# Kernel tuning notes

Hardware: AMD Instinct MI355X
Metric: run time of the kernel (lower is better)

Reference implementation:

```python
import jax, jax.numpy as jnp
import numpy as np

N = 100000      # num nodes
E = 3200000     # num edges
F = 128         # feature dim (in == out, required by final in-place copy)
U = 1000        # num_users


def gcn_conv(x, edge_index, W, b):
    """PyG GCNConv: symmetric-normalized adjacency with self-loops.
    out = D^{-1/2} (A + I) D^{-1/2} X W + b
    """
    xw = x @ W                                   # [N, F]
    src, dst = edge_index[0], edge_index[1]
    # in-degree including the self-loop (+1)
    deg = jax.ops.segment_sum(jnp.ones((E,), x.dtype), dst, num_segments=N) + 1.0
    inv_sqrt = jax.lax.rsqrt(deg)                # [N]
    coef = inv_sqrt[src] * inv_sqrt[dst]         # [E]
    agg = jax.ops.segment_sum(xw[src] * coef[:, None], dst, num_segments=N)
    # self-loop contribution: norm_ii = inv_sqrt[i]^2
    return agg + xw * (inv_sqrt * inv_sqrt)[:, None] + b


def setup_inputs() -> dict:
    key = jax.random.key(0)
    k1, k2, k3, k4, k5, k6 = jax.random.split(key, 6)
    x = jax.random.normal(k1, (N, F), dtype=jnp.float32)
    edge_index = jax.random.randint(k2, (2, E), 0, N, dtype=jnp.int64)
    s = 1.0 / np.sqrt(F)
    W1 = jax.random.normal(k3, (F, F), dtype=jnp.float32) * s
    b1 = jnp.zeros((F,), dtype=jnp.float32)
    W2 = jax.random.normal(k4, (F, F), dtype=jnp.float32) * s
    b2 = jnp.zeros((F,), dtype=jnp.float32)
    return {"x": x, "edge_index": edge_index, "W1": W1, "b1": b1, "W2": W2, "b2": b2}


def reference(x, edge_index, W1, b1, W2, b2):
    # eval mode: dropout(p=0.5, training=False) is identity; detach is a no-op in fwd
    h = jax.nn.elu(gcn_conv(x, edge_index, W1, b1))
    h = jax.nn.elu(gcn_conv(h, edge_index, W2, b2))
    # x[num_users:] = movie_features  -> movie rows restored to original input
    return jnp.concatenate([h[:U], x[U:]], axis=0)
```

## Files before the change

### kernel.cpp

```cpp
#include <hip/hip_runtime.h>


#define F_DIM 128
#define U_USERS 1000
#define NFCAP 48000
#define HW 25008
#define PSLICE 128
#define BMW 3136
#define SMEM_BYTES 32768
#define NBPS 49

using f16x8 = __attribute__((ext_vector_type(8))) _Float16;
using f16x2 = __attribute__((ext_vector_type(2))) _Float16;
using f32x4 = __attribute__((ext_vector_type(4))) float;
using i32x4 = __attribute__((ext_vector_type(4))) int;

__global__ __launch_bounds__(256) void zero_kernel(int* __restrict__ fr,
                                                   unsigned long long* __restrict__ desc,
                                                   int n) {
    int t = blockIdx.x * 256 + threadIdx.x;
    int n4 = n >> 2;
    if (t < n4) ((int4*)fr)[t] = make_int4(0, 0, 0, 0);
    if (t < (n & 3)) fr[(n & ~3) + t] = 0;
    if (t < NBPS) desc[t] = 0ull;
}

__global__ __launch_bounds__(1024) void hist_kernel(const int* __restrict__ src,
                                                    const int* __restrict__ dst,
                                                    unsigned int* __restrict__ partial,
                                                    int* __restrict__ fr, int E, int n) {
    __shared__ unsigned int h[HW];
    int tid = threadIdx.x;
    int p = blockIdx.x;
    for (int i = tid; i < HW; i += 1024) h[i] = 0u;
    __syncthreads();

    int len = (E + PSLICE - 1) / PSLICE;
    int base = p * len;
    int end = min(E, base + len);
    int e = base + tid * 4;
    for (; e + 3 < end; e += 4096) {
        i32x4 dv = __builtin_nontemporal_load((const i32x4*)(dst + e));
#pragma unroll
        for (int i = 0; i < 4; ++i) {
            int d = dv[i];
            if ((unsigned)d < (unsigned)n) {
                atomicAdd(&h[d >> 2], 1u << ((d & 3) << 3));
                if (d < U_USERS) {
                    int s = src[e + i];
                    if ((unsigned)s < (unsigned)n) fr[s] = 1;
                }
            }
        }
    }
    for (; e < end; ++e) {
        int d = dst[e];
        if ((unsigned)d < (unsigned)n) {
            atomicAdd(&h[d >> 2], 1u << ((d & 3) << 3));
            if (d < U_USERS) {
                int s = src[e];
                if ((unsigned)s < (unsigned)n) fr[s] = 1;
            }
        }
    }
    __syncthreads();
    unsigned int* outp = partial + (size_t)p * HW;
    for (int i = tid; i < HW; i += 1024) outp[i] = h[i];
}

__global__ __launch_bounds__(1024) void prep_scan_kernel(
    const unsigned int* __restrict__ partial, const int* __restrict__ fr,
    float* __restrict__ inv, int* __restrict__ rp, int* __restrict__ remap,
    int* __restrict__ flist, int* __restrict__ nf_dev,
    unsigned int* __restrict__ bitsG, unsigned long long* __restrict__ desc, int n) {
    __shared__ unsigned long long ss[1024];
    __shared__ unsigned int bmw[64];
    __shared__ unsigned long long spre;
    int b = blockIdx.x, t = threadIdx.x;
    int i0 = b * 2048 + t * 2;
    bool in0 = i0 < n, in1 = i0 + 1 < n;

    unsigned a0 = 0, a1 = 0;
    if (in0) {
        int w = i0 >> 2;
        int sh = (i0 & 2) * 8;
        const unsigned int* bp = partial + w;
#pragma unroll 8
        for (int p = 0; p < PSLICE; ++p) {
            unsigned v = bp[(size_t)p * HW];
            a0 += (v >> sh) & 0xFFu;
            a1 += (v >> (sh + 8)) & 0xFFu;
        }
    }
    int fv0 = 0, fv1 = 0;
    if (in1) { int2 f2 = *(const int2*)(fr + i0); fv0 = f2.x; fv1 = f2.y; }
    else if (in0) fv0 = fr[i0];
    int isf0 = (in0 && ((i0 < U_USERS) || fv0)) ? 1 : 0;
    int isf1 = (in1 && ((i0 + 1 < U_USERS) || fv1)) ? 1 : 0;
    unsigned d0 = isf0 ? a0 : 0u, d1 = isf1 ? a1 : 0u;

    float r0v = rsqrtf((float)a0 + 1.f);
    float r1v = rsqrtf((float)a1 + 1.f);
    if (in1) *(float2*)(inv + i0) = make_float2(r0v, r1v);
    else if (in0) inv[i0] = r0v;

    if (t < 64) bmw[t] = 0u;
    __syncthreads();
    unsigned pbits = (unsigned)isf0 | ((unsigned)isf1 << 1);
    if (pbits) atomicOr(&bmw[(t * 2) >> 5], pbits << ((t * 2) & 31));
    __syncthreads();
    if (t < 64) bitsG[b * 64 + t] = bmw[t];

    unsigned long long myv = ((unsigned long long)(d0 + d1) << 20) |
                             (unsigned)(isf0 + isf1);
    ss[t] = myv;
    __syncthreads();
    for (int ofs = 1; ofs < 1024; ofs <<= 1) {
        unsigned long long v = (t >= ofs) ? ss[t - ofs] : 0ull;
        __syncthreads(); ss[t] += v; __syncthreads();
    }
    unsigned long long total = ss[1023];

    if (t == 0) atomicExch(&desc[b], (total << 1) | 1ull);
    if (t < 64) {
        int pblk = b - 1 - t;
        unsigned long long v = 0ull;
        if (pblk >= 0) {
            unsigned long long d;
            do { d = atomicAdd(&desc[pblk], 0ull); } while (!(d & 1ull));
            v = d >> 1;
        }
#pragma unroll
        for (int o = 32; o > 0; o >>= 1) v += __shfl_down(v, o);
        if (t == 0) spre = v;
    }
    __syncthreads();

    unsigned long long ex = spre + ss[t] - myv;
    int rp0 = (int)(ex >> 20), rm0 = (int)(ex & 0xFFFFFu);
    unsigned long long ex1 = ex + ((((unsigned long long)d0) << 20) | (unsigned)isf0);
    int rp1 = (int)(ex1 >> 20), rm1 = (int)(ex1 & 0xFFFFFu);
    if (in1) {
        *(int2*)(rp + i0) = make_int2(rp0, rp1);
        *(int2*)(remap + i0) = make_int2(rm0, rm1);
    } else if (in0) { rp[i0] = rp0; remap[i0] = rm0; }
    if (isf0 && rm0 < NFCAP) flist[rm0] = i0;
    if (isf1 && rm1 < NFCAP) flist[rm1] = i0 + 1;
    if (in0 && i0 == n - 1) *nf_dev = min(rm0 + isf0, NFCAP);
    if (in1 && i0 + 1 == n - 1) *nf_dev = min(rm1 + isf1, NFCAP);
}

__device__ __forceinline__ void fill_csr_body(const int* __restrict__ src,
                                              const int* __restrict__ dst,
                                              const unsigned int* __restrict__ bitsG,
                                              int* __restrict__ rp, int* __restrict__ col,
                                              int E, int n, int fblk,
                                              unsigned char* smem) {
    unsigned int* bm = (unsigned int*)smem;
    int tid = threadIdx.x;
    int nw = (n + 31) >> 5;
    for (int i = tid; i < nw; i += 256) bm[i] = bitsG[i];
    __syncthreads();

    int t = fblk * 256 + tid;
    int e0 = t * 4;
    if (e0 + 3 < E) {
        i32x4 dv = __builtin_nontemporal_load((const i32x4*)(dst + e0));
        i32x4 sv = __builtin_nontemporal_load((const i32x4*)(src + e0));
        bool f[4];
#pragma unroll
        for (int i = 0; i < 4; ++i) {
            int d = dv[i];
            f[i] = ((unsigned)d < (unsigned)n) && ((unsigned)sv[i] < (unsigned)n)
                   && ((bm[d >> 5] >> (d & 31)) & 1u);
        }
        int pos[4];
#pragma unroll
        for (int i = 0; i < 4; ++i) {
            pos[i] = -1;
            if (f[i]) pos[i] = atomicAdd(&rp[dv[i]], 1);
        }
#pragma unroll
        for (int i = 0; i < 4; ++i) {
            if (f[i] && (unsigned)pos[i] < (unsigned)E) col[pos[i]] = sv[i];
        }
    } else {
        for (int e = e0; e < E; ++e) {
            int d = dst[e], s = src[e];
            if ((unsigned)d < (unsigned)n && (unsigned)s < (unsigned)n &&
                ((bm[d >> 5] >> (d & 31)) & 1u)) {
                int pos = atomicAdd(&rp[d], 1);
                if ((unsigned)pos < (unsigned)E) col[pos] = s;
            }
        }
    }
}

__device__ __forceinline__ void stage_wt(const float* __restrict__ W, _Float16* Wt, int tid) {
#pragma unroll
    for (int i = 0; i < 8; ++i) {
        int j = tid + 256 * i;
        int nr = j & 127;
        int k8 = j >> 7;
        f16x8 v;
#pragma unroll
        for (int kk = 0; kk < 8; ++kk)
            v[kk] = (_Float16)W[(k8 * 8 + kk) * F_DIM + nr];
        *(f16x8*)&Wt[nr * F_DIM + ((k8 ^ (nr & 15)) * 8)] = v;
    }
}

__device__ __forceinline__ void gemm_mfma_body(const float* __restrict__ X,
                                               const float* __restrict__ W,
                                               unsigned char* __restrict__ out8,
                                               float* __restrict__ pout,
                                               int nrows, int rowBase,
                                               unsigned char* smem) {
    _Float16* Wt = (_Float16*)smem;
    int tid = threadIdx.x;
    stage_wt(W, Wt, tid);
    __syncthreads();

    int w = tid >> 6;
    int lane = tid & 63;
    int m = lane & 15;
    int quad = lane >> 4;
    int row = rowBase + w * 16 + m;
    bool rv = row < nrows;

    f16x8 a0, a1, a2, a3;
    {
        const float* xr = X + (size_t)row * F_DIM;
        float* pr = (pout != nullptr && rv && row >= U_USERS)
                        ? pout + (size_t)row * F_DIM : nullptr;
#pragma unroll
        for (int kc = 0; kc < 4; ++kc) {
            f32x4 lo = (f32x4){0.f, 0.f, 0.f, 0.f};
            f32x4 hi = lo;
            if (rv) {
                lo = __builtin_nontemporal_load((const f32x4*)(xr + kc * 32 + quad * 8));
                hi = __builtin_nontemporal_load((const f32x4*)(xr + kc * 32 + quad * 8) + 1);
            }
            if (pr) {
                __builtin_nontemporal_store(lo, (f32x4*)(pr + kc * 32 + quad * 8));
                __builtin_nontemporal_store(hi, (f32x4*)(pr + kc * 32 + quad * 8) + 1);
            }
            f16x8 av;
            av[0] = (_Float16)lo[0]; av[1] = (_Float16)lo[1];
            av[2] = (_Float16)lo[2]; av[3] = (_Float16)lo[3];
            av[4] = (_Float16)hi[0]; av[5] = (_Float16)hi[1];
            av[6] = (_Float16)hi[2]; av[7] = (_Float16)hi[3];
            if (kc == 0) a0 = av; else if (kc == 1) a1 = av;
            else if (kc == 2) a2 = av; else a3 = av;
        }
    }

    f32x4 acc[8];
#pragma unroll
    for (int i = 0; i < 8; ++i) acc[i] = (f32x4){0.f, 0.f, 0.f, 0.f};

#pragma unroll
    for (int kc = 0; kc < 4; ++kc) {
        f16x8 a = (kc == 0) ? a0 : (kc == 1) ? a1 : (kc == 2) ? a2 : a3;
#pragma unroll
        for (int ct = 0; ct < 8; ++ct) {
            f16x8 b = *(const f16x8*)&Wt[(ct * 16 + m) * F_DIM +
                                         (((kc * 4 + quad) ^ m) * 8)];
            acc[ct] = __builtin_amdgcn_mfma_f32_16x16x32_f16(a, b, acc[ct], 0, 0, 0);
        }
    }

#pragma unroll
    for (int ct = 0; ct < 8; ++ct) {
#pragma unroll
        for (int reg = 0; reg < 4; ++reg) {
            int r = rowBase + w * 16 + quad * 4 + reg;
            if (r < nrows) {
                float v = acc[ct][reg];
                int p8 = __builtin_amdgcn_cvt_pk_fp8_f32(v, v, 0, false);
                out8[(size_t)r * F_DIM + ct * 16 + m] = (unsigned char)(p8 & 0xFF);
            }
        }
    }
}

__device__ __forceinline__ void gemm_mfma_body_h(const _Float16* __restrict__ Xh,
                                                 const float* __restrict__ W,
                                                 _Float16* __restrict__ outh,
                                                 int nrows, int rowBase,
                                                 unsigned char* smem) {
    _Float16* Wt = (_Float16*)smem;
    int tid = threadIdx.x;
    stage_wt(W, Wt, tid);
    __syncthreads();

    int w = tid >> 6;
    int lane = tid & 63;
    int m = lane & 15;
    int quad = lane >> 4;
    int row = rowBase + w * 16 + m;
    const _Float16* xr = Xh + (size_t)row * F_DIM;

    f32x4 acc[8];
#pragma unroll
    for (int i = 0; i < 8; ++i) acc[i] = (f32x4){0.f, 0.f, 0.f, 0.f};

#pragma unroll
    for (int kc = 0; kc < 4; ++kc) {
        f16x8 a = *(const f16x8*)(xr + kc * 32 + quad * 8);
#pragma unroll
        for (int ct = 0; ct < 8; ++ct) {
            f16x8 b = *(const f16x8*)&Wt[(ct * 16 + m) * F_DIM +
                                         (((kc * 4 + quad) ^ m) * 8)];
            acc[ct] = __builtin_amdgcn_mfma_f32_16x16x32_f16(a, b, acc[ct], 0, 0, 0);
        }
    }

#pragma unroll
    for (int ct = 0; ct < 8; ++ct) {
#pragma unroll
        for (int reg = 0; reg < 4; ++reg) {
            int r = rowBase + w * 16 + quad * 4 + reg;
            if (r < nrows)
                outh[(size_t)r * F_DIM + ct * 16 + m] = (_Float16)acc[ct][reg];
        }
    }
}

__global__ __launch_bounds__(256) void gemm_fill_kernel(const float* __restrict__ X,
                                                        const float* __restrict__ W,
                                                        unsigned char* __restrict__ out8,
                                                        float* __restrict__ pout, int nrows,
                                                        int gemmBlocks, int totalBlocks,
                                                        const int* __restrict__ src,
                                                        const int* __restrict__ dst,
                                                        const unsigned int* __restrict__ bitsG,
                                                        int* __restrict__ rp,
                                                        int* __restrict__ col, int E, int n) {
    __shared__ __align__(16) unsigned char smem[SMEM_BYTES];
    int b = blockIdx.x;
    long long g = gemmBlocks, T = totalBlocks;
    int before = (int)((long long)b * g / T);
    int after  = (int)(((long long)b + 1) * g / T);
    if (after > before) {
        gemm_mfma_body(X, W, out8, pout, nrows, before * 64, smem);
    } else {
        fill_csr_body(src, dst, bitsG, rp, col, E, n, b - before, smem);
    }
}

__global__ __launch_bounds__(256) void gemm_f16_dyn_kernel(const _Float16* __restrict__ Xh,
                                                           const float* __restrict__ W,
                                                           _Float16* __restrict__ outh,
                                                           const int* __restrict__ nrows_p) {
    __shared__ __align__(16) unsigned char smem[SMEM_BYTES];
    int nrows = *nrows_p;
    int rowBase = blockIdx.x * 64;
    if (rowBase >= nrows) return;
    gemm_mfma_body_h(Xh, W, outh, nrows, rowBase, smem);
}

__global__ __launch_bounds__(256) void gather_l1_kernel(const unsigned char* __restrict__ xw8,
                                                        const float* __restrict__ inv,
                                                        const int* __restrict__ rp,
                                                        const int* __restrict__ col,
                                                        const int* __restrict__ flist,
                                                        const int* __restrict__ nf_p,
                                                        const float* __restrict__ b,
                                                        _Float16* __restrict__ h1c) {
    int ci = blockIdx.x * 4 + (threadIdx.x >> 6);
    if (ci >= *nf_p) return;
    int lane = threadIdx.x & 63;
    int node = flist[ci];
    int start = (node == 0) ? 0 : rp[node - 1];
    int end = rp[node];

    float accx = 0.f, accy = 0.f;
    for (int base = start; base < end; base += 64) {
        int j = base + lane;
        int s_l = 0; float c_l = 0.f;
        if (j < end) { s_l = __builtin_nontemporal_load(col + j); c_l = inv[s_l]; }
        int cnt = min(64, end - base);
        int i = 0;
        for (; i + 8 <= cnt; i += 8) {
            int ss[8]; float ff[8]; unsigned short vv[8];
#pragma unroll
            for (int u = 0; u < 8; ++u) { ss[u] = __shfl(s_l, i + u); ff[u] = __shfl(c_l, i + u); }
#pragma unroll
            for (int u = 0; u < 8; ++u)
                vv[u] = ((const unsigned short*)(xw8 + (size_t)ss[u] * F_DIM))[lane];
#pragma unroll
            for (int u = 0; u < 8; ++u) {
                accx += __builtin_amdgcn_cvt_f32_fp8((int)vv[u], 0) * ff[u];
                accy += __builtin_amdgcn_cvt_f32_fp8((int)vv[u], 1) * ff[u];
            }
        }
        for (; i + 4 <= cnt; i += 4) {
            int ss[4]; float ff[4]; unsigned short vv[4];
#pragma unroll
            for (int u = 0; u < 4; ++u) { ss[u] = __shfl(s_l, i + u); ff[u] = __shfl(c_l, i + u); }
#pragma unroll
            for (int u = 0; u < 4; ++u)
                vv[u] = ((const unsigned short*)(xw8 + (size_t)ss[u] * F_DIM))[lane];
#pragma unroll
            for (int u = 0; u < 4; ++u) {
                accx += __builtin_amdgcn_cvt_f32_fp8((int)vv[u], 0) * ff[u];
                accy += __builtin_amdgcn_cvt_f32_fp8((int)vv[u], 1) * ff[u];
            }
        }
        for (; i < cnt; ++i) {
            int s0 = __shfl(s_l, i); float f0 = __shfl(c_l, i);
            unsigned short v0 = ((const unsigned short*)(xw8 + (size_t)s0 * F_DIM))[lane];
            accx += __builtin_amdgcn_cvt_f32_fp8((int)v0, 0) * f0;
            accy += __builtin_amdgcn_cvt_f32_fp8((int)v0, 1) * f0;
        }
    }

    float ivd = inv[node];
    unsigned short selfraw = ((const unsigned short*)(xw8 + (size_t)node * F_DIM))[lane];
    float s0 = __builtin_amdgcn_cvt_f32_fp8((int)selfraw, 0);
    float s1 = __builtin_amdgcn_cvt_f32_fp8((int)selfraw, 1);
    float vx = accx * ivd + s0 * ivd * ivd + b[lane * 2];
    float vy = accy * ivd + s1 * ivd * ivd + b[lane * 2 + 1];
    vx = vx > 0.f ? vx : expf(vx) - 1.f;
    vy = vy > 0.f ? vy : expf(vy) - 1.f;
    f16x2 o; o[0] = (_Float16)vx; o[1] = (_Float16)vy;
    ((f16x2*)(h1c + (size_t)ci * F_DIM))[lane] = o;
}

__global__ __launch_bounds__(256) void gather_l2_kernel(const _Float16* __restrict__ xwc,
                                                        const float* __restrict__ inv,
                                                        const int* __restrict__ rp,
                                                        const int* __restrict__ col,
                                                        const int* __restrict__ remap,
                                                        const float* __restrict__ b,
                                                        float* __restrict__ out) {
    int node = blockIdx.x * 4 + (threadIdx.x >> 6);
    if (node >= U_USERS) return;
    int lane = threadIdx.x & 63;
    int start = (node == 0) ? 0 : rp[node - 1];
    int end = rp[node];

    float accx = 0.f, accy = 0.f;
    for (int base = start; base < end; base += 64) {
        int j = base + lane;
        int r_l = 0; float c_l = 0.f;
        if (j < end) { int s = __builtin_nontemporal_load(col + j); c_l = inv[s]; r_l = remap[s]; }
        int cnt = min(64, end - base);
        int i = 0;
        for (; i + 8 <= cnt; i += 8) {
            int rr[8]; float ff[8]; f16x2 vv[8];
#pragma unroll
            for (int u = 0; u < 8; ++u) { rr[u] = __shfl(r_l, i + u); ff[u] = __shfl(c_l, i + u); }
#pragma unroll
            for (int u = 0; u < 8; ++u) vv[u] = ((const f16x2*)(xwc + (size_t)rr[u] * F_DIM))[lane];
#pragma unroll
            for (int u = 0; u < 8; ++u) { accx += (float)vv[u][0] * ff[u]; accy += (float)vv[u][1] * ff[u]; }
        }
        for (; i + 4 <= cnt; i += 4) {
            int rr[4]; float ff[4]; f16x2 vv[4];
#pragma unroll
            for (int u = 0; u < 4; ++u) { rr[u] = __shfl(r_l, i + u); ff[u] = __shfl(c_l, i + u); }
#pragma unroll
            for (int u = 0; u < 4; ++u) vv[u] = ((const f16x2*)(xwc + (size_t)rr[u] * F_DIM))[lane];
#pragma unroll
            for (int u = 0; u < 4; ++u) { accx += (float)vv[u][0] * ff[u]; accy += (float)vv[u][1] * ff[u]; }
        }
        for (; i < cnt; ++i) {
            int r0 = __shfl(r_l, i); float f0 = __shfl(c_l, i);
            f16x2 v0 = ((const f16x2*)(xwc + (size_t)r0 * F_DIM))[lane];
            accx += (float)v0[0] * f0;
            accy += (float)v0[1] * f0;
        }
    }

    float ivd = inv[node];
    f16x2 self = ((const f16x2*)(xwc + (size_t)node * F_DIM))[lane];
    float vx = accx * ivd + (float)self[0] * ivd * ivd + b[lane * 2];
    float vy = accy * ivd + (float)self[1] * ivd * ivd + b[lane * 2 + 1];
    vx = vx > 0.f ? vx : expf(vx) - 1.f;
    vy = vy > 0.f ? vy : expf(vy) - 1.f;
    ((float2*)(out + (size_t)node * F_DIM))[lane] = make_float2(vx, vy);
}

extern "C" void kernel_launch(void* const* d_in, const int* in_sizes, int n_in,
                              void* d_out, int out_size, void* d_ws, size_t ws_size,
                              hipStream_t stream) {
    const float* x  = (const float*)d_in[0];
    const int*   ei = (const int*)d_in[1];
    const float* W1 = (const float*)d_in[2];
    const float* b1 = (const float*)d_in[3];
    const float* W2 = (const float*)d_in[4];
    const float* b2 = (const float*)d_in[5];
    float* out = (float*)d_out;

    int n = in_sizes[0] / F_DIM;
    int E = in_sizes[1] / 2;
    const int* srcI = ei;
    const int* dstI = ei + E;

    unsigned char* xw8 = (unsigned char*)d_ws;
    _Float16* xwc = (_Float16*)(xw8 + (size_t)n * F_DIM);
    _Float16* h1c = xwc + (size_t)NFCAP * F_DIM;
    float* inv   = (float*)(h1c + (size_t)NFCAP * F_DIM);
    int* fr      = (int*)(inv + n);
    int* remap   = fr + n;
    int* rp      = remap + n;
    int* flist   = rp + n;
    int* nf_dev  = flist + NFCAP;
    int* col     = nf_dev + 16;
    unsigned int* partialH = (unsigned int*)(col + E);
    unsigned int* bitsG = partialH + (size_t)PSLICE * HW;
    unsigned long long* desc = (unsigned long long*)(bitsG + BMW);

    zero_kernel<<<(n / 4 + 255) / 256, 256, 0, stream>>>(fr, desc, n);

    hist_kernel<<<PSLICE, 1024, 0, stream>>>(srcI, dstI, partialH, fr, E, n);

    prep_scan_kernel<<<NBPS, 1024, 0, stream>>>(partialH, fr, inv, rp, remap,
                                                flist, nf_dev, bitsG, desc, n);

    int fillBlocks = (E / 4 + 255) / 256;
    int gemmBlocks = (n + 63) / 64;
    gemm_fill_kernel<<<fillBlocks + gemmBlocks, 256, 0, stream>>>(
        x, W1, xw8, out, n, gemmBlocks, fillBlocks + gemmBlocks,
        srcI, dstI, bitsG, rp, col, E, n);

    gather_l1_kernel<<<(NFCAP + 3) / 4, 256, 0, stream>>>(xw8, inv, rp, col, flist, nf_dev, b1, h1c);

    gemm_f16_dyn_kernel<<<(NFCAP + 63) / 64, 256, 0, stream>>>(h1c, W2, xwc, nf_dev);
    gather_l2_kernel<<<(U_USERS + 3) / 4, 256, 0, stream>>>(xwc, inv, rp, col, remap, b2, out);
}
```

Baseline: 247.4 us.

## Replace global-atomic CSR fill with per-slice prefix bases and LDS rank counters

The prep scan now writes a per-slice base offset for each frontier node from the per-slice histograms. A new 128-block fill kernel replays each edge slice and takes ranks from shared-memory byte counters instead of global atomics on rp. This yields a deterministic CSR with exclusive row pointers (rp[n] added). The fused gemm+fill launch is split into separate kernels, which removes the overlap between GEMM and fill. The prep kernel also does extra serial work per frontier node to write 128 bases.

```diff
diff --git a/kernel.cpp b/kernel.cpp
--- a/kernel.cpp
+++ b/kernel.cpp
@@ -72,7 +72,8 @@
     const unsigned int* __restrict__ partial, const int* __restrict__ fr,
     float* __restrict__ inv, int* __restrict__ rp, int* __restrict__ remap,
     int* __restrict__ flist, int* __restrict__ nf_dev,
-    unsigned int* __restrict__ bitsG, unsigned long long* __restrict__ desc, int n) {
+    unsigned int* __restrict__ bitsG, unsigned int* __restrict__ baseF,
+    unsigned long long* __restrict__ desc, int n) {
     __shared__ unsigned long long ss[1024];
     __shared__ unsigned int bmw[64];
     __shared__ unsigned long long spre;
@@ -148,49 +149,82 @@
     if (isf1 && rm1 < NFCAP) flist[rm1] = i0 + 1;
     if (in0 && i0 == n - 1) *nf_dev = min(rm0 + isf0, NFCAP);
     if (in1 && i0 + 1 == n - 1) *nf_dev = min(rm1 + isf1, NFCAP);
-}
-
-__device__ __forceinline__ void fill_csr_body(const int* __restrict__ src,
-                                              const int* __restrict__ dst,
-                                              const unsigned int* __restrict__ bitsG,
-                                              int* __restrict__ rp, int* __restrict__ col,
-                                              int E, int n, int fblk,
-                                              unsigned char* smem) {
-    unsigned int* bm = (unsigned int*)smem;
+    if (b == NBPS - 1 && t == 1023) rp[n] = (int)((spre + total) >> 20);
+
+    if (isf0 && rm0 < NFCAP) {
+        unsigned run = (unsigned)rp0;
+        const unsigned int* bp = partial + (i0 >> 2);
+        int sh0 = (i0 & 3) << 3;
+        unsigned int* bf = baseF + (size_t)rm0 * PSLICE;
+#pragma unroll 8
+        for (int p = 0; p < PSLICE; ++p) {
+            bf[p] = run;
+            run += (bp[(size_t)p * HW] >> sh0) & 0xFFu;
+        }
+    }
+    if (isf1 && rm1 < NFCAP) {
+        unsigned run = (unsigned)rp1;
+        const unsigned int* bp = partial + ((i0 + 1) >> 2);
+        int sh1 = ((i0 + 1) & 3) << 3;
+        unsigned int* bf = baseF + (size_t)rm1 * PSLICE;
+#pragma unroll 8
+        for (int p = 0; p < PSLICE; ++p) {
+            bf[p] = run;
+            run += (bp[(size_t)p * HW] >> sh1) & 0xFFu;
+        }
+    }
+}
+
+__global__ __launch_bounds__(1024) void fill_csr_kernel(const int* __restrict__ src,
+                                                        const int* __restrict__ dst,
+                                                        const unsigned int* __restrict__ bitsG,
+                                                        const int* __restrict__ remap,
+                                                        const unsigned int* __restrict__ baseF,
+                                                        int* __restrict__ col, int E, int n) {
+    __shared__ unsigned int bm[BMW];
+    __shared__ unsigned int cnt[12288];
     int tid = threadIdx.x;
-    int nw = (n + 31) >> 5;
-    for (int i = tid; i < nw; i += 256) bm[i] = bitsG[i];
-    __syncthreads();
-
-    int t = fblk * 256 + tid;
-    int e0 = t * 4;
-    if (e0 + 3 < E) {
-        i32x4 dv = __builtin_nontemporal_load((const i32x4*)(dst + e0));
-        i32x4 sv = __builtin_nontemporal_load((const i32x4*)(src + e0));
-        bool f[4];
+    int p = blockIdx.x;
+    for (int i = tid; i < BMW; i += 1024) bm[i] = bitsG[i];
+    for (int i = tid; i < 12288; i += 1024) cnt[i] = 0u;
+    __syncthreads();
+
+    int len = (E + PSLICE - 1) / PSLICE;
+    int base = p * len;
+    int end = min(E, base + len);
+    int e = base + tid * 4;
+    for (; e + 3 < end; e += 4096) {
+        i32x4 dv = __builtin_nontemporal_load((const i32x4*)(dst + e));
+        i32x4 sv = __builtin_nontemporal_load((const i32x4*)(src + e));
 #pragma unroll
         for (int i = 0; i < 4; ++i) {
             int d = dv[i];
-            f[i] = ((unsigned)d < (unsigned)n) && ((unsigned)sv[i] < (unsigned)n)
-                   && ((bm[d >> 5] >> (d & 31)) & 1u);
-        }
-        int pos[4];
-#pragma unroll
-        for (int i = 0; i < 4; ++i) {
-            pos[i] = -1;
-            if (f[i]) pos[i] = atomicAdd(&rp[dv[i]], 1);
-        }
-#pragma unroll
-        for (int i = 0; i < 4; ++i) {
-            if (f[i] && (unsigned)pos[i] < (unsigned)E) col[pos[i]] = sv[i];
-        }
-    } else {
-        for (int e = e0; e < E; ++e) {
-            int d = dst[e], s = src[e];
-            if ((unsigned)d < (unsigned)n && (unsigned)s < (unsigned)n &&
-                ((bm[d >> 5] >> (d & 31)) & 1u)) {
-                int pos = atomicAdd(&rp[d], 1);
-                if ((unsigned)pos < (unsigned)E) col[pos] = s;
+            if (((unsigned)d < (unsigned)n) && ((bm[d >> 5] >> (d & 31)) & 1u)) {
+                int f = remap[d];
+                if ((unsigned)f < (unsigned)NFCAP) {
+                    unsigned bs = baseF[(size_t)f * PSLICE + p];
+                    int sh = (f & 3) << 3;
+                    unsigned old = atomicAdd(&cnt[f >> 2], 1u << sh);
+                    unsigned rank = (old >> sh) & 0xFFu;
+                    unsigned pos = bs + rank;
+                    int s = sv[i];
+                    if (pos < (unsigned)E) col[pos] = ((unsigned)s < (unsigned)n) ? s : 0;
+                }
+            }
+        }
+    }
+    for (; e < end; ++e) {
+        int d = dst[e];
+        if (((unsigned)d < (unsigned)n) && ((bm[d >> 5] >> (d & 31)) & 1u)) {
+            int f = remap[d];
+            if ((unsigned)f < (unsigned)NFCAP) {
+                unsigned bs = baseF[(size_t)f * PSLICE + p];
+                int sh = (f & 3) << 3;
+                unsigned old = atomicAdd(&cnt[f >> 2], 1u << sh);
+                unsigned rank = (old >> sh) & 0xFFu;
+                unsigned pos = bs + rank;
+                int s = src[e];
+                if (pos < (unsigned)E) col[pos] = ((unsigned)s < (unsigned)n) ? s : 0;
             }
         }
     }
@@ -210,14 +244,14 @@
     }
 }
 
-__device__ __forceinline__ void gemm_mfma_body(const float* __restrict__ X,
-                                               const float* __restrict__ W,
-                                               unsigned char* __restrict__ out8,
-                                               float* __restrict__ pout,
-                                               int nrows, int rowBase,
-                                               unsigned char* smem) {
+__global__ __launch_bounds__(256) void gemm_f16_kernel(const float* __restrict__ X,
+                                                       const float* __restrict__ W,
+                                                       unsigned char* __restrict__ out8,
+                                                       float* __restrict__ pout, int nrows) {
+    __shared__ __align__(16) unsigned char smem[SMEM_BYTES];
     _Float16* Wt = (_Float16*)smem;
     int tid = threadIdx.x;
+    int rowBase = blockIdx.x * 64;
     stage_wt(W, Wt, tid);
     __syncthreads();
 
@@ -231,8 +265,7 @@
     f16x8 a0, a1, a2, a3;
     {
         const float* xr = X + (size_t)row * F_DIM;
-        float* pr = (pout != nullptr && rv && row >= U_USERS)
-                        ? pout + (size_t)row * F_DIM : nullptr;
+        float* pr = (rv && row >= U_USERS) ? pout + (size_t)row * F_DIM : nullptr;
 #pragma unroll
         for (int kc = 0; kc < 4; ++kc) {
             f32x4 lo = (f32x4){0.f, 0.f, 0.f, 0.f};
@@ -284,12 +317,15 @@
     }
 }
 
-__device__ __forceinline__ void gemm_mfma_body_h(const _Float16* __restrict__ Xh,
-                                                 const float* __restrict__ W,
-                                                 _Float16* __restrict__ outh,
-                                                 int nrows, int rowBase,
-                                                 unsigned char* smem) {
+__global__ __launch_bounds__(256) void gemm_f16_dyn_kernel(const _Float16* __restrict__ Xh,
+                                                           const float* __restrict__ W,
+                                                           _Float16* __restrict__ outh,
+                                                           const int* __restrict__ nrows_p) {
+    __shared__ __align__(16) unsigned char smem[SMEM_BYTES];
     _Float16* Wt = (_Float16*)smem;
+    int nrows = *nrows_p;
+    int rowBase = blockIdx.x * 64;
+    if (rowBase >= nrows) return;
     int tid = threadIdx.x;
     stage_wt(W, Wt, tid);
     __syncthreads();
@@ -325,39 +361,6 @@
                 outh[(size_t)r * F_DIM + ct * 16 + m] = (_Float16)acc[ct][reg];
         }
     }
-}
-
-__global__ __launch_bounds__(256) void gemm_fill_kernel(const float* __restrict__ X,
-                                                        const float* __restrict__ W,
-                                                        unsigned char* __restrict__ out8,
-                                                        float* __restrict__ pout, int nrows,
-                                                        int gemmBlocks, int totalBlocks,
-                                                        const int* __restrict__ src,
-                                                        const int* __restrict__ dst,
-                                                        const unsigned int* __restrict__ bitsG,
-                                                        int* __restrict__ rp,
-                                                        int* __restrict__ col, int E, int n) {
-    __shared__ __align__(16) unsigned char smem[SMEM_BYTES];
-    int b = blockIdx.x;
-    long long g = gemmBlocks, T = totalBlocks;
-    int before = (int)((long long)b * g / T);
-    int after  = (int)(((long long)b + 1) * g / T);
-    if (after > before) {
-        gemm_mfma_body(X, W, out8, pout, nrows, before * 64, smem);
-    } else {
-        fill_csr_body(src, dst, bitsG, rp, col, E, n, b - before, smem);
-    }
-}
-
-__global__ __launch_bounds__(256) void gemm_f16_dyn_kernel(const _Float16* __restrict__ Xh,
-                                                           const float* __restrict__ W,
-                                                           _Float16* __restrict__ outh,
-                                                           const int* __restrict__ nrows_p) {
-    __shared__ __align__(16) unsigned char smem[SMEM_BYTES];
-    int nrows = *nrows_p;
-    int rowBase = blockIdx.x * 64;
-    if (rowBase >= nrows) return;
-    gemm_mfma_body_h(Xh, W, outh, nrows, rowBase, smem);
 }
 
 __global__ __launch_bounds__(256) void gather_l1_kernel(const unsigned char* __restrict__ xw8,
@@ -372,8 +375,8 @@
     if (ci >= *nf_p) return;
     int lane = threadIdx.x & 63;
     int node = flist[ci];
-    int start = (node == 0) ? 0 : rp[node - 1];
-    int end = rp[node];
+    int start = rp[node];
+    int end = rp[node + 1];
 
     float accx = 0.f, accy = 0.f;
     for (int base = start; base < end; base += 64) {
@@ -438,8 +441,8 @@
     int node = blockIdx.x * 4 + (threadIdx.x >> 6);
     if (node >= U_USERS) return;
     int lane = threadIdx.x & 63;
-    int start = (node == 0) ? 0 : rp[node - 1];
-    int end = rp[node];
+    int start = rp[node];
+    int end = rp[node + 1];
 
     float accx = 0.f, accy = 0.f;
     for (int base = start; base < end; base += 64) {
@@ -506,25 +509,24 @@
     int* fr      = (int*)(inv + n);
     int* remap   = fr + n;
     int* rp      = remap + n;
-    int* flist   = rp + n;
+    int* flist   = rp + n + 16;
     int* nf_dev  = flist + NFCAP;
     int* col     = nf_dev + 16;
     unsigned int* partialH = (unsigned int*)(col + E);
     unsigned int* bitsG = partialH + (size_t)PSLICE * HW;
     unsigned long long* desc = (unsigned long long*)(bitsG + BMW);
+    unsigned int* baseF = (unsigned int*)(desc + NBPS + 7);
 
     zero_kernel<<<(n / 4 + 255) / 256, 256, 0, stream>>>(fr, desc, n);
 
     hist_kernel<<<PSLICE, 1024, 0, stream>>>(srcI, dstI, partialH, fr, E, n);
 
     prep_scan_kernel<<<NBPS, 1024, 0, stream>>>(partialH, fr, inv, rp, remap,
-                                                flist, nf_dev, bitsG, desc, n);
-
-    int fillBlocks = (E / 4 + 255) / 256;
-    int gemmBlocks = (n + 63) / 64;
-    gemm_fill_kernel<<<fillBlocks + gemmBlocks, 256, 0, stream>>>(
-        x, W1, xw8, out, n, gemmBlocks, fillBlocks + gemmBlocks,
-        srcI, dstI, bitsG, rp, col, E, n);
+                                                flist, nf_dev, bitsG, baseF, desc, n);
+
+    fill_csr_kernel<<<PSLICE, 1024, 0, stream>>>(srcI, dstI, bitsG, remap, baseF, col, E, n);
+
+    gemm_f16_kernel<<<(n + 63) / 64, 256, 0, stream>>>(x, W1, xw8, out, n);
 
     gather_l1_kernel<<<(NFCAP + 3) / 4, 256, 0, stream>>>(xw8, inv, rp, col, flist, nf_dev, b1, h1c);
 
```

After: 299.8 us. +21.1%, slower.
